# Performance work log

Hardware: AMD Instinct MI355X
Metric: run time of the kernel (lower is better)

## Reference

```python
import jax, jax.numpy as jnp
import numpy as np

T, N, E = 4, 20000, 320000
F_IN, EH, NH, GH, OUT = 12, 32, 64, 64, 1
NUM_LAYERS = 2
EB_IN = (EH + 2 * NH) * 2 + GH  # 384
NB_IN = 2 * NH + 2 * EH + GH    # 256
GB_IN = NH + EH + GH            # 160


def setup_inputs() -> dict:
    key = jax.random.key(0)
    ks = jax.random.split(key, 24)
    f32 = jnp.float32
    def w(k, fan_in, shape):
        return jax.random.normal(k, shape, f32) * (1.0 / np.sqrt(fan_in))
    return {
        "node_attr": jax.random.normal(ks[0], (T, N, F_IN), f32),
        "edge_attr": jax.random.normal(ks[1], (T, E, 1), f32),
        "edge_index": jax.random.randint(ks[2], (2, E), 0, N, jnp.int32),
        "sp_L_vals": jax.random.normal(ks[3], (E,), f32),
        "global_attr": jax.random.normal(ks[4], (1, GH), f32),
        "coeff": jnp.full((1,), 0.1, f32),
        "W_ee": w(ks[5], 1, (1, EH)), "b_ee": jnp.zeros((EH,), f32),
        "W_ne": w(ks[6], F_IN, (F_IN, NH)), "b_ne": jnp.zeros((NH,), f32),
        "W_eb": w(ks[7], EB_IN, (EB_IN, EH)), "b_eb": jnp.zeros((EH,), f32),
        "W_nb": w(ks[8], NB_IN, (NB_IN, NH)), "b_nb": jnp.zeros((NH,), f32),
        "W_gb": w(ks[9], GB_IN, (GB_IN, GH)), "b_gb": jnp.zeros((GH,), f32),
        "W_nd1": w(ks[10], NH, (NH, NH)), "b_nd1": jnp.zeros((NH,), f32),
        "W_nd2": w(ks[11], NH, (NH, OUT)), "b_nd2": jnp.zeros((OUT,), f32),
    }


def _forward(node_attr, edge_attr, edge_index, sp_L_vals, global_attr, coeff,
             W_ee, b_ee, W_ne, b_ne, W_eb, b_eb, W_nb, b_nb, W_gb, b_gb,
             W_nd1, b_nd1, W_nd2, b_nd2):
    relu = jax.nn.relu
    s, r = edge_index[0], edge_index[1]
    seg = lambda v, idx: jax.ops.segment_sum(v, idx, num_segments=N)
    c = coeff[0]

    # encoders
    x_enc = relu(node_attr @ W_ne + b_ne)   # [T,N,NH]
    e_enc = relu(edge_attr @ W_ee + b_ee)   # [T,E,EH]

    def run_gn(xT, eT, g0):
        # recurrent GN core over processing steps; hidden (h_x,h_e,h_g) starts at zeros
        def step(carry, inp):
            h_x, h_e, h_g = carry
            x_in, e_in = inp
            gE = jnp.broadcast_to(h_g, (E, GH))
            # EdgeBlock: [edge_in, edge_h, sender_in, sender_h, recv_in, recv_h, global]
            edge_cat = jnp.concatenate(
                [e_in, h_e, x_in[s], h_x[s], x_in[r], h_x[r], gE], axis=-1)
            e_new = relu(edge_cat @ W_eb + b_eb)              # [E,EH]
            sent = seg(e_new, s)                              # scatter_add by sender
            recv = seg(e_new, r)                              # scatter_add by receiver
            gN = jnp.broadcast_to(h_g, (N, GH))
            node_cat = jnp.concatenate([x_in, h_x, sent, recv, gN], axis=-1)
            x_new = relu(node_cat @ W_nb + b_nb)              # [N,NH]
            # GlobalBlock: scatter_mean == plain mean (single graph)
            g_cat = jnp.concatenate(
                [x_new.mean(0, keepdims=True), e_new.mean(0, keepdims=True), h_g], axis=-1)
            g_new = relu(g_cat @ W_gb + b_gb)                 # [1,GH]
            # physics terms (pde='diff'): time derivative = state update,
            # spatial derivative = coeff * (graph-Laplacian action via sp_L edge weights)
            t_der = x_new - h_x
            s_der = c * seg(sp_L_vals[:, None] * (x_new[s] - x_new[r]), r)
            return (x_new, e_new, g_new), (x_new, e_new, g_new, t_der, s_der)
        carry0 = (jnp.zeros((N, NH), jnp.float32), jnp.zeros((E, EH), jnp.float32), g0)
        _, ys = jax.lax.scan(step, carry0, (xT, eT))
        return ys  # xs[T,N,NH], es[T,E,EH], gs[T,1,GH], td[T,N,NH], sd[T,N,NH]

    xs, es, gs, td, sd = run_gn(x_enc, e_enc, global_attr)
    x_pre = x_enc
    for _ in range(NUM_LAYERS - 1):
        x_res = xs + x_pre          # residual node state feeds next GN layer
        x_pre = x_res
        xs, es, gs, td, sd = run_gn(x_res, es, gs[0])

    x_final = xs + x_pre            # add_residual=True final residual
    h = relu(x_final @ W_nd1 + b_nd1)
    out_nodes = h @ W_nd2 + b_nd2   # [T,N,OUT]
    return out_nodes, td, sd


def reference(node_attr, edge_attr, edge_index, sp_L_vals, global_attr, coeff,
              W_ee, b_ee, W_ne, b_ne, W_eb, b_eb, W_nb, b_nb, W_gb, b_gb,
              W_nd1, b_nd1, W_nd2, b_nd2):
    return _forward(node_attr, edge_attr, edge_index, sp_L_vals, global_attr, coeff,
                    W_ee, b_ee, W_ne, b_ne, W_eb, b_eb, W_nb, b_nb, W_gb, b_gb,
                    W_nd1, b_nd1, W_nd2, b_nd2)
```

## Files before the change

kernel.cpp:

```cpp
#include <hip/hip_runtime.h>


typedef __attribute__((ext_vector_type(8))) short s16x8;
typedef __attribute__((ext_vector_type(4))) float f32x4;

#define T_STEPS 4
#define NN 20000
#define NP 20224
#define NE 320000

__device__ __forceinline__ float bf2f(unsigned short h){
  return __uint_as_float(((unsigned)h)<<16);
}
__device__ __forceinline__ unsigned short f2bf(float f){
  unsigned u = __float_as_uint(f);
  return (unsigned short)((u + 0x7fffu + ((u>>16)&1u)) >> 16);
}
__device__ __forceinline__ float loadIn(const void* p, size_t i, int bf){
  return bf ? bf2f(((const unsigned short*)p)[i]) : ((const float*)p)[i];
}
__device__ __forceinline__ void storeOut(void* o, size_t i, float v, int bf){
  if(bf) ((unsigned short*)o)[i] = f2bf(v);
  else   ((float*)o)[i] = v;
}
__device__ __forceinline__ void load8(const float* __restrict__ p, float* v){
  const float4* q4 = (const float4*)p;
  float4 a = q4[0], b = q4[1];
  v[0]=a.x; v[1]=a.y; v[2]=a.z; v[3]=a.w;
  v[4]=b.x; v[5]=b.y; v[6]=b.z; v[7]=b.w;
}
__device__ __forceinline__ int4 pack8(const float* v){
  unsigned p0 = (unsigned)f2bf(v[0]) | ((unsigned)f2bf(v[1])<<16);
  unsigned p1 = (unsigned)f2bf(v[2]) | ((unsigned)f2bf(v[3])<<16);
  unsigned p2 = (unsigned)f2bf(v[4]) | ((unsigned)f2bf(v[5])<<16);
  unsigned p3 = (unsigned)f2bf(v[6]) | ((unsigned)f2bf(v[7])<<16);
  return make_int4((int)p0,(int)p1,(int)p2,(int)p3);
}
__device__ __forceinline__ void unp8(int4 w, float* a){
  unsigned x;
  x=(unsigned)w.x; a[0]=__uint_as_float(x<<16); a[1]=__uint_as_float(x&0xffff0000u);
  x=(unsigned)w.y; a[2]=__uint_as_float(x<<16); a[3]=__uint_as_float(x&0xffff0000u);
  x=(unsigned)w.z; a[4]=__uint_as_float(x<<16); a[5]=__uint_as_float(x&0xffff0000u);
  x=(unsigned)w.w; a[6]=__uint_as_float(x<<16); a[7]=__uint_as_float(x&0xffff0000u);
}

union I4S8 { int4 i; s16x8 s; };

struct ConvJob { const void* src; float* dst; int n; };
struct ConvJobs { ConvJob j[16]; int cnt; };

__global__ void conv_kernel(ConvJobs jobs, const void* coeff_in, int* flagp,
                            float* coeff_f, float* z, int zn){
  unsigned short u = ((const unsigned short*)coeff_in)[0];
  float as_bf = bf2f(u);
  int bf = (fabsf(as_bf - 0.1f) < 0.02f) ? 1 : 0;
  int tid = blockIdx.x*blockDim.x + threadIdx.x;
  if(tid==0){ *flagp = bf; *coeff_f = bf ? as_bf : ((const float*)coeff_in)[0]; }
  int stride = gridDim.x*blockDim.x;
  for(int q=0;q<jobs.cnt;q++){
    const void* s = jobs.j[q].src; float* d = jobs.j[q].dst; int n = jobs.j[q].n;
    for(int i=tid;i<n;i+=stride) d[i] = loadIn(s, i, bf);
  }
  for(int i=tid;i<zn;i+=stride) z[i]=0.f;
}

__global__ void csr_hist(const int* __restrict__ ei, int* deg_s, int* deg_r,
                         unsigned short* __restrict__ rank_s,
                         unsigned short* __restrict__ rank_r){
  int e = blockIdx.x*256+threadIdx.x;
  rank_s[e] = (unsigned short)atomicAdd(&deg_s[ei[e]],1);
  rank_r[e] = (unsigned short)atomicAdd(&deg_r[ei[NE+e]],1);
}

__global__ void csr_scan(const int* __restrict__ deg_s, int* __restrict__ off_s,
                         const int* __restrict__ deg_r, int* __restrict__ off_r){
  const int CH = NP/256;
  const int* deg = blockIdx.x ? deg_r : deg_s;
  int* off = blockIdx.x ? off_r : off_s;
  int t = threadIdx.x;
  int base = t*CH;
  int s = 0;
  #pragma unroll 8
  for(int i=0;i<CH;i++) s += deg[base+i];
  int lane = t & 63, w = t >> 6;
  int x = s;
  #pragma unroll
  for(int o=1;o<64;o<<=1){
    int y = __shfl_up(x, o, 64);
    if(lane >= o) x += y;
  }
  __shared__ int wtot[4];
  if(lane==63) wtot[w] = x;
  __syncthreads();
  int wbase = 0;
  #pragma unroll
  for(int k=0;k<3;k++) if(k<w) wbase += wtot[k];
  int acc = wbase + x - s;
  #pragma unroll 8
  for(int i=0;i<CH;i++){
    off[base+i]=acc; acc+=deg[base+i];
  }
  if(t==255) off[NN]=acc;
}

__global__ void fill_pack_enc_kernel(
  const int* __restrict__ ei,
  const int* __restrict__ s_off, const int* __restrict__ r_off,
  const unsigned short* __restrict__ rank_s,
  const unsigned short* __restrict__ rank_r,
  int* __restrict__ csr_s, int* __restrict__ csr_r, int2* __restrict__ sr2,
  const void* __restrict__ spL, float* __restrict__ spL_p,
  const void* __restrict__ W_eb_in, const void* __restrict__ W_nb_in,
  const void* __restrict__ W_nd1_in,
  unsigned short* __restrict__ WpE, unsigned short* __restrict__ WpN,
  unsigned short* __restrict__ WpD, unsigned short* __restrict__ WpP,
  const void* __restrict__ na, const float* __restrict__ W_ne,
  const float* __restrict__ b_ne, unsigned short* __restrict__ xA,
  const int* flagp)
{
  __shared__ float arow[4][12];
  const int blk = blockIdx.x;
  const int bf = *flagp;
  if(blk < NE/256){
    int e = blk*256+threadIdx.x;
    int s = ei[e], r = ei[NE+e];
    int p = r_off[r] + rank_r[e];
    sr2[p] = make_int2(s,r);
    csr_r[p] = e;
    csr_s[s_off[s]+rank_s[e]] = p;
    spL_p[p] = loadIn(spL, e, bf);
  } else if(blk < NE/256 + 120){
    int idx = (blk - NE/256)*256 + threadIdx.x;
    if(idx < 22528){
      const void* W; unsigned short* P; int KW, NT;
      if(idx < 2048){ W=W_eb_in; P=WpE; KW=2; NT=2; }
      else if(idx < 18432){ idx -= 2048; W=W_nb_in; P=WpN; KW=8; NT=4; }
      else { idx -= 18432; W=W_nd1_in; P=WpD; KW=2; NT=4; }
      int j = idx & 7;
      int lane = (idx>>3) & 63;
      int rest = idx >> 9;
      int kw = rest % KW;
      int nt = rest / KW;
      int k = kw*32 + (lane>>4)*8 + j;
      int n = nt*16 + (lane&15);
      P[idx] = f2bf(loadIn(W, (size_t)k*(NT*16) + n, bf));
    } else {
      int idx2 = idx - 22528;
      int j = idx2 & 7;
      int lane = (idx2>>3) & 63;
      int rest = idx2 >> 9;
      int kw = rest & 3;
      int nt = rest >> 2;
      int row = (nt<2 ? 64 : 192) + kw*32 + (lane>>4)*8 + j;
      int col = (nt&1)*16 + (lane&15);
      WpP[idx2] = f2bf(loadIn(W_eb_in, (size_t)row*32 + col, bf));
    }
  } else {
    int lane = threadIdx.x & 63, nl = threadIdx.x >> 6;
    int row = (blk - (NE/256 + 120))*4 + nl;
    if(lane<12) arow[nl][lane] = loadIn(na, (size_t)row*12+lane, bf);
    __syncthreads();
    float acc = b_ne[lane];
    #pragma unroll
    for(int k=0;k<12;k++) acc += arow[nl][k]*W_ne[k*64+lane];
    xA[(size_t)row*64+lane] = f2bf(fmaxf(acc,0.f));
  }
}

__global__ __launch_bounds__(256) void node_pre_kernel(
  const unsigned short* __restrict__ x_in,
  const unsigned short* __restrict__ h_x,
  const unsigned short* __restrict__ WpP,
  const float* __restrict__ g,
  const void* __restrict__ W_eb_in, const float* __restrict__ b_eb,
  float* __restrict__ srT, float* __restrict__ gbias,
  const int* flagp)
{
  const int tid = threadIdx.x, lane = tid&63;
  const int q = lane>>4, m16 = lane&15;
  if(blockIdx.x >= 313){
    if(tid < 32){
      int bf = *flagp;
      float gb = b_eb[tid];
      for(int k=0;k<64;k++){
        float gv = bf2f(f2bf(g[k]));
        float wv = bf2f(f2bf(loadIn(W_eb_in, (size_t)(320+k)*32 + tid, bf)));
        gb += gv*wv;
      }
      gbias[tid] = gb;
    }
    return;
  }
  const int tile = blockIdx.x*4 + (tid>>6);
  if(tile >= NN/16) return;
  const int n0 = tile*16, ng = n0+m16;
  const int4 z4 = make_int4(0,0,0,0);
  I4S8 A[4];
  { const int4* xp = (const int4*)(x_in + (size_t)ng*64);
    A[0].i = xp[q]; A[1].i = xp[4+q]; }
  if(h_x){ const int4* hp = (const int4*)(h_x + (size_t)ng*64);
    A[2].i = hp[q]; A[3].i = hp[4+q];
  } else { A[2].i = z4; A[3].i = z4; }
  f32x4 acc[4];
  #pragma unroll
  for(int nt=0;nt<4;nt++) acc[nt] = (f32x4){0.f,0.f,0.f,0.f};
  #pragma unroll
  for(int kw=0;kw<4;kw++){
    #pragma unroll
    for(int nt=0;nt<4;nt++){
      s16x8 b = *(const s16x8*)(WpP + (size_t)((nt*4+kw)*64 + lane)*8);
      acc[nt] = __builtin_amdgcn_mfma_f32_16x16x32_bf16(A[kw].s, b, acc[nt], 0,0,0);
    }
  }
  #pragma unroll
  for(int r=0;r<4;r++){
    int n = n0 + q*4 + r;
    #pragma unroll
    for(int nt=0;nt<4;nt++)
      srT[(size_t)n*64 + nt*16 + m16] = acc[nt][r];
  }
}

__global__ __launch_bounds__(256) void edge_block_mfma(
  const int2* __restrict__ sr2,
  const void* __restrict__ e_attr,
  int e_attr_off,
  const int* __restrict__ inv,
  const unsigned short* __restrict__ e_in,
  const unsigned short* __restrict__ h_e,
  const float* __restrict__ W_ee, const float* __restrict__ b_ee,
  const unsigned short* __restrict__ Wp,
  const float* __restrict__ srT,
  const float* __restrict__ gbias,
  unsigned short* __restrict__ e_out,
  float* __restrict__ partial_e,
  const int* flagp)
{
  const int tid = threadIdx.x;
  const int lane = tid&63;
  const int q = lane>>4, m16 = lane&15;
  const int pair = blockIdx.x*4 + (tid>>6);
  const int e0 = pair*32;
  const int eg0 = e0 + m16, eg1 = e0 + 16 + m16;
  const int o8 = q*8;
  const int4 z4 = make_int4(0,0,0,0);

  I4S8 A0[2], A1[2];
  if(e_attr){
    int bf = *flagp;
    float a0v = loadIn(e_attr, (size_t)e_attr_off + inv[eg0], bf);
    float a1v = loadIn(e_attr, (size_t)e_attr_off + inv[eg1], bf);
    float v[8];
    #pragma unroll
    for(int j=0;j<8;j++) v[j] = fmaxf(a0v*W_ee[o8+j]+b_ee[o8+j], 0.f);
    A0[0].i = pack8(v);
    #pragma unroll
    for(int j=0;j<8;j++) v[j] = fmaxf(a1v*W_ee[o8+j]+b_ee[o8+j], 0.f);
    A1[0].i = pack8(v);
  } else {
    A0[0].i = ((const int4*)(e_in + (size_t)eg0*32))[q];
    A1[0].i = ((const int4*)(e_in + (size_t)eg1*32))[q];
  }
  A0[1].i = h_e ? ((const int4*)(h_e + (size_t)eg0*32))[q] : z4;
  A1[1].i = h_e ? ((const int4*)(h_e + (size_t)eg1*32))[q] : z4;

  f32x4 a00={0.f,0.f,0.f,0.f}, a01={0.f,0.f,0.f,0.f};
  f32x4 a10={0.f,0.f,0.f,0.f}, a11={0.f,0.f,0.f,0.f};
  #pragma unroll
  for(int kw=0;kw<2;kw++){
    s16x8 b0 = *(const s16x8*)(Wp + (size_t)(kw*64 + lane)*8);
    s16x8 b1 = *(const s16x8*)(Wp + (size_t)((2+kw)*64 + lane)*8);
    a00 = __builtin_amdgcn_mfma_f32_16x16x32_bf16(A0[kw].s, b0, a00, 0,0,0);
    a01 = __builtin_amdgcn_mfma_f32_16x16x32_bf16(A0[kw].s, b1, a01, 0,0,0);
    a10 = __builtin_amdgcn_mfma_f32_16x16x32_bf16(A1[kw].s, b0, a10, 0,0,0);
    a11 = __builtin_amdgcn_mfma_f32_16x16x32_bf16(A1[kw].s, b1, a11, 0,0,0);
  }

  const float gb0 = gbias[m16], gb1 = gbias[16+m16];
  int2 rw[8];
  #pragma unroll
  for(int r=0;r<4;r++){
    rw[r]   = sr2[e0 + q*4 + r];
    rw[4+r] = sr2[e0 + 16 + q*4 + r];
  }
  float sv0[8], sv1[8], rv0[8], rv1[8];
  #pragma unroll
  for(int k=0;k<8;k++){
    sv0[k] = srT[(size_t)rw[k].x*64 + m16];
    sv1[k] = srT[(size_t)rw[k].x*64 + 16 + m16];
    rv0[k] = srT[(size_t)rw[k].y*64 + 32 + m16];
    rv1[k] = srT[(size_t)rw[k].y*64 + 48 + m16];
  }

  float pe0=0.f, pe1=0.f;
  #pragma unroll
  for(int r=0;r<4;r++){
    int eg0m = e0 + q*4 + r;
    int eg1m = eg0m + 16;
    float v00 = fmaxf(a00[r] + sv0[r]   + rv0[r]   + gb0, 0.f);
    float v01 = fmaxf(a01[r] + sv1[r]   + rv1[r]   + gb1, 0.f);
    float v10 = fmaxf(a10[r] + sv0[4+r] + rv0[4+r] + gb0, 0.f);
    float v11 = fmaxf(a11[r] + sv1[4+r] + rv1[4+r] + gb1, 0.f);
    e_out[(size_t)eg0m*32+m16]    = f2bf(v00);
    e_out[(size_t)eg0m*32+16+m16] = f2bf(v01);
    e_out[(size_t)eg1m*32+m16]    = f2bf(v10);
    e_out[(size_t)eg1m*32+16+m16] = f2bf(v11);
    pe0 += v00+v10; pe1 += v01+v11;
  }
  pe0 += __shfl_xor(pe0,16,64); pe0 += __shfl_xor(pe0,32,64);
  pe1 += __shfl_xor(pe1,16,64); pe1 += __shfl_xor(pe1,32,64);
  if(q==0){
    int slot = blockIdx.x & 63;
    atomicAdd(&partial_e[slot*32+m16],    pe0);
    atomicAdd(&partial_e[slot*32+16+m16], pe1);
  }
}

__global__ void aggregate_kernel(const unsigned short* __restrict__ e_new,
  const int* __restrict__ s_off, const int* __restrict__ csr_s,
  const int* __restrict__ r_off,
  unsigned short* __restrict__ sentB, unsigned short* __restrict__ recvB)
{
  int node = blockIdx.x*4 + (threadIdx.x>>6);
  int lane = threadIdx.x & 63;
  int c4 = (lane & 7) * 4;
  int jr = lane >> 3;
  float s0=0.f,s1=0.f,s2=0.f,s3=0.f;
  float r0=0.f,r1=0.f,r2=0.f,r3=0.f;
  {
    int beg = s_off[node], end = s_off[node+1];
    for(int i=beg+jr; i<end; i+=8){
      uint2 w = *(const uint2*)(e_new + (size_t)csr_s[i]*32 + c4);
      s0 += __uint_as_float(w.x<<16);
      s1 += __uint_as_float(w.x&0xffff0000u);
      s2 += __uint_as_float(w.y<<16);
      s3 += __uint_as_float(w.y&0xffff0000u);
    }
  }
  {
    int beg = r_off[node], end = r_off[node+1];
    for(int i=beg+jr; i<end; i+=8){
      uint2 w = *(const uint2*)(e_new + (size_t)i*32 + c4);
      r0 += __uint_as_float(w.x<<16);
      r1 += __uint_as_float(w.x&0xffff0000u);
      r2 += __uint_as_float(w.y<<16);
      r3 += __uint_as_float(w.y&0xffff0000u);
    }
  }
  #pragma unroll
  for(int o=8;o<64;o<<=1){
    s0 += __shfl_xor(s0,o,64); s1 += __shfl_xor(s1,o,64);
    s2 += __shfl_xor(s2,o,64); s3 += __shfl_xor(s3,o,64);
    r0 += __shfl_xor(r0,o,64); r1 += __shfl_xor(r1,o,64);
    r2 += __shfl_xor(r2,o,64); r3 += __shfl_xor(r3,o,64);
  }
  if(jr==0){
    unsigned slo = (unsigned)f2bf(s0) | ((unsigned)f2bf(s1)<<16);
    unsigned shi = (unsigned)f2bf(s2) | ((unsigned)f2bf(s3)<<16);
    unsigned rlo = (unsigned)f2bf(r0) | ((unsigned)f2bf(r1)<<16);
    unsigned rhi = (unsigned)f2bf(r2) | ((unsigned)f2bf(r3)<<16);
    *(uint2*)(sentB + (size_t)node*32 + c4) = make_uint2(slo,shi);
    *(uint2*)(recvB + (size_t)node*32 + c4) = make_uint2(rlo,rhi);
  }
}

__global__ __launch_bounds__(256) void node_block_mfma(
  const unsigned short* __restrict__ x_in, const unsigned short* __restrict__ h_x,
  const unsigned short* __restrict__ sentB, const unsigned short* __restrict__ recvB,
  const float* __restrict__ g,
  const unsigned short* __restrict__ Wp,
  const float* __restrict__ b_nb,
  unsigned short* __restrict__ x_out,
  unsigned short* __restrict__ xres_out,
  float* __restrict__ partial_x,
  void* __restrict__ out_base, size_t td_off, int has_td,
  float* __restrict__ partial_e,
  const float* __restrict__ W_gb, const float* __restrict__ b_gb,
  float* __restrict__ g_out, int* __restrict__ cnt,
  const int* flagp)
{
  __shared__ int lastFlag;
  __shared__ float gcat[160];
  __shared__ float red[4][64];
  const int tid = threadIdx.x, lane = tid&63;
  const int q = lane>>4, m16 = lane&15;
  const int tile = blockIdx.x*4 + (tid>>6);
  if(tile < NN/16){
    const int n0 = tile*16;
    const int ng = n0+m16;
    const int o8 = q*8;
    const int4 z4 = make_int4(0,0,0,0);

    I4S8 A[8];
    { const int4* xp = (const int4*)(x_in + (size_t)ng*64);
      A[0].i = xp[q]; A[1].i = xp[4+q]; }
    if(h_x){ const int4* hp = (const int4*)(h_x + (size_t)ng*64);
      A[2].i = hp[q]; A[3].i = hp[4+q];
    } else { A[2].i = z4; A[3].i = z4; }
    A[4].i = ((const int4*)(sentB + (size_t)ng*32))[q];
    A[5].i = ((const int4*)(recvB + (size_t)ng*32))[q];
    { float v[8];
      load8(g + o8, v);      A[6].i = pack8(v);
      load8(g + 32 + o8, v); A[7].i = pack8(v); }

    f32x4 acc[4];
    #pragma unroll
    for(int nt=0;nt<4;nt++) acc[nt] = (f32x4){0.f,0.f,0.f,0.f};
    #pragma unroll
    for(int kw=0;kw<8;kw++){
      #pragma unroll
      for(int nt=0;nt<4;nt++){
        s16x8 b = *(const s16x8*)(Wp + (size_t)((nt*8+kw)*64 + lane)*8);
        acc[nt] = __builtin_amdgcn_mfma_f32_16x16x32_bf16(A[kw].s, b, acc[nt], 0,0,0);
      }
    }

    int bf = has_td ? *flagp : 0;
    float ps[4] = {0.f,0.f,0.f,0.f};
    #pragma unroll
    for(int r=0;r<4;r++){
      int nodeg = n0 + q*4 + r;
      #pragma unroll
      for(int nt=0;nt<4;nt++){
        int col = nt*16 + m16;
        float vv = fmaxf(acc[nt][r] + b_nb[col], 0.f);
        unsigned short hb = f2bf(vv);
        x_out[(size_t)nodeg*64+col] = hb;
        if(xres_out){
          float xv = bf2f(x_in[(size_t)nodeg*64+col]);
          xres_out[(size_t)nodeg*64+col] = f2bf(xv + bf2f(hb));
        }
        if(has_td){
          float hxv = h_x ? bf2f(h_x[(size_t)nodeg*64+col]) : 0.f;
          storeOut(out_base, td_off + (size_t)nodeg*64+col, vv - hxv, bf);
        }
        ps[nt] += vv;
      }
    }
    #pragma unroll
    for(int nt=0;nt<4;nt++){
      ps[nt] += __shfl_xor(ps[nt],16,64);
      ps[nt] += __shfl_xor(ps[nt],32,64);
    }
    if(q==0){
      int slot = blockIdx.x & 63;
      #pragma unroll
      for(int nt=0;nt<4;nt++)
        atomicAdd(&partial_x[slot*64 + nt*16 + m16], ps[nt]);
    }
  }

  asm volatile("s_waitcnt vmcnt(0)" ::: "memory");
  __syncthreads();
  if(tid==0) lastFlag = (atomicAdd(cnt,1) == (int)gridDim.x - 1) ? 1 : 0;
  __syncthreads();
  if(!lastFlag) return;

  if(tid<64){
    float sx = 0.f;
    #pragma unroll 8
    for(int i=0;i<64;i++)
      sx += __hip_atomic_load(&partial_x[i*64+tid], __ATOMIC_RELAXED, __HIP_MEMORY_SCOPE_AGENT);
    gcat[tid] = sx * (1.0f/(float)NN);
  } else if(tid<96){
    int j = tid-64;
    float se = 0.f;
    #pragma unroll 8
    for(int i=0;i<64;i++)
      se += __hip_atomic_load(&partial_e[i*32+j], __ATOMIC_RELAXED, __HIP_MEMORY_SCOPE_AGENT);
    gcat[64+j] = se * (1.0f/(float)NE);
  } else if(tid<160){
    gcat[tid] = g[tid-96];
  }
  __syncthreads();
  int j = tid&63, cc = tid>>6;
  float acc2 = 0.f;
  #pragma unroll 8
  for(int k=cc*40;k<cc*40+40;k++) acc2 += gcat[k]*W_gb[k*64+j];
  red[cc][j] = acc2;
  __syncthreads();
  for(int i=tid;i<2048;i+=256) partial_e[i]=0.f;
  for(int i=tid;i<4096;i+=256) partial_x[i]=0.f;
  if(tid<64){
    float a = red[0][tid]+red[1][tid]+red[2][tid]+red[3][tid] + b_gb[tid];
    g_out[tid] = fmaxf(a, 0.f);
  }
  if(tid==0) *cnt = 0;
}

__global__ void sder_csr_kernel(const int2* __restrict__ sr2,
  const float* __restrict__ spL_p, const unsigned short* __restrict__ x_new,
  const int* __restrict__ r_off,
  const float* __restrict__ coeff, void* __restrict__ out_base, size_t off,
  const int* flagp)
{
  int bf = *flagp;
  int lane = threadIdx.x&63, nl = threadIdx.x>>6;
  int node = blockIdx.x*4+nl;
  float xn = bf2f(x_new[(size_t)node*64+lane]);
  float a0=0.f, a1=0.f, a2=0.f, a3=0.f;
  int beg = r_off[node], end = r_off[node+1];
  int i = beg;
  for(; i+4<=end; i+=4){
    float w1 = spL_p[i],   w2 = spL_p[i+1];
    float w3 = spL_p[i+2], w4 = spL_p[i+3];
    int s1 = sr2[i].x, s2 = sr2[i+1].x, s3 = sr2[i+2].x, s4 = sr2[i+3].x;
    a0 += w1*(bf2f(x_new[(size_t)s1*64+lane])-xn);
    a1 += w2*(bf2f(x_new[(size_t)s2*64+lane])-xn);
    a2 += w3*(bf2f(x_new[(size_t)s3*64+lane])-xn);
    a3 += w4*(bf2f(x_new[(size_t)s4*64+lane])-xn);
  }
  for(; i<end; i++){
    float w1 = spL_p[i];
    a0 += w1*(bf2f(x_new[(size_t)sr2[i].x*64+lane])-xn);
  }
  storeOut(out_base, off + (size_t)node*64+lane, coeff[0]*((a0+a1)+(a2+a3)), bf);
}

__global__ __launch_bounds__(256) void decoder_kernel(
  const unsigned short* __restrict__ xs, const unsigned short* __restrict__ xr,
  const unsigned short* __restrict__ WpD,
  const float* __restrict__ b1, const float* __restrict__ W2,
  const float* __restrict__ b2,
  void* __restrict__ out_base, const int* flagp)
{
  const int tid=threadIdx.x, lane=tid&63;
  const int q=lane>>4, m16=lane&15;
  const int tile = blockIdx.x*4 + (tid>>6);
  const int row0 = tile*16;
  const int rg = row0 + m16;

  I4S8 A[2];
  #pragma unroll
  for(int kw=0;kw<2;kw++){
    int4 xa = ((const int4*)(xs + (size_t)rg*64 + kw*32))[q];
    int4 xb = ((const int4*)(xr + (size_t)rg*64 + kw*32))[q];
    float va[8], vb[8], v[8];
    unp8(xa, va); unp8(xb, vb);
    #pragma unroll
    for(int j=0;j<8;j++) v[j] = va[j]+vb[j];
    A[kw].i = pack8(v);
  }

  f32x4 acc[4];
  #pragma unroll
  for(int nt=0;nt<4;nt++) acc[nt] = (f32x4){0.f,0.f,0.f,0.f};
  #pragma unroll
  for(int kw=0;kw<2;kw++){
    #pragma unroll
    for(int nt=0;nt<4;nt++){
      s16x8 b = *(const s16x8*)(WpD + (size_t)((nt*2+kw)*64 + lane)*8);
      acc[nt] = __builtin_amdgcn_mfma_f32_16x16x32_bf16(A[kw].s, b, acc[nt], 0,0,0);
    }
  }

  float val[4];
  #pragma unroll
  for(int r=0;r<4;r++){
    float s = 0.f;
    #pragma unroll
    for(int nt=0;nt<4;nt++){
      int col = nt*16 + m16;
      s += fmaxf(acc[nt][r] + b1[col], 0.f) * W2[col];
    }
    val[r] = s;
  }
  #pragma unroll
  for(int o=1;o<16;o<<=1){
    #pragma unroll
    for(int r=0;r<4;r++) val[r] += __shfl_xor(val[r], o, 64);
  }
  if(m16==0){
    int bf = *flagp;
    float bb = b2[0];
    #pragma unroll
    for(int r=0;r<4;r++)
      storeOut(out_base, (size_t)(row0 + q*4 + r), val[r] + bb, bf);
  }
}

extern "C" void kernel_launch(void* const* d_in, const int* in_sizes, int n_in,
                              void* d_out, int out_size, void* d_ws, size_t ws_size,
                              hipStream_t stream){
  const void* node_attr = d_in[0];
  const void* edge_attr = d_in[1];
  const int*  ei        = (const int*)d_in[2];
  const void* spL       = d_in[3];
  const void* gattr     = d_in[4];
  const void* coeff_in  = d_in[5];
  const void* W_ee_in = d_in[6];  const void* b_ee_in = d_in[7];
  const void* W_ne_in = d_in[8];  const void* b_ne_in = d_in[9];
  const void* W_eb_in = d_in[10]; const void* b_eb_in = d_in[11];
  const void* W_nb_in = d_in[12]; const void* b_nb_in = d_in[13];
  const void* W_gb_in = d_in[14]; const void* b_gb_in = d_in[15];
  const void* W_nd1_in= d_in[16]; const void* b_nd1_in= d_in[17];
  const void* W_nd2_in= d_in[18]; const void* b_nd2_in= d_in[19];

  float* ws = (float*)d_ws;
  float* W_ee_f = ws;             float* b_ee_f = W_ee_f+32;
  float* W_ne_f = b_ee_f+32;      float* b_ne_f = W_ne_f+768;
  float* W_gb_f = b_ne_f+64;      float* b_gb_f = W_gb_f+10240;
  float* W_nd1_f= b_gb_f+64;      float* b_nd1_f= W_nd1_f+4096;
  float* W_nd2_f= b_nd1_f+64;     float* b_nd2_f= W_nd2_f+64;
  float* b_eb_f = b_nd2_f+1;      float* b_nb_f = b_eb_f+32;
  float* coeff_f= b_nb_f+64;
  int*   flagp  = (int*)(ws + 15523);
  float* gbuf   = ws + 15524;
  float* zbase  = ws + 16100;
  int*   cnt    = (int*)zbase;
  float* part_e = zbase + 4;
  float* part_x = part_e + 2048;
  int*   deg_s  = (int*)(part_x + 4096);
  int*   deg_r  = deg_s + NP;
  int*   s_off  = deg_r + NP;
  int*   r_off  = s_off + NP+1;
  unsigned short* rank_s = (unsigned short*)(r_off + NP+1);
  unsigned short* rank_r = rank_s + NE;
  int*   csr_s  = (int*)(rank_r + NE);
  int*   csr_r  = csr_s + NE;
  float* spL_p  = (float*)(csr_r + NE);
  size_t iend   = (size_t)((int*)(spL_p + NE) - (int*)ws);
  iend = (iend + 3) & ~(size_t)3;
  int2*  sr2    = (int2*)(ws + iend);
  unsigned short* sentB = (unsigned short*)(sr2 + NE);
  unsigned short* recvB = sentB + (size_t)NN*32;
  unsigned short* eBuf  = recvB + (size_t)NN*32;
  unsigned short* xA    = eBuf + (size_t)T_STEPS*NE*32;
  unsigned short* xB    = xA + (size_t)T_STEPS*NN*64;
  unsigned short* xC    = xB + (size_t)T_STEPS*NN*64;
  unsigned short* WpE   = xC + (size_t)T_STEPS*NN*64;
  unsigned short* WpN   = WpE + 2048;
  unsigned short* WpD   = WpN + 16384;
  unsigned short* WpP   = WpD + 4096;
  float* srT   = (float*)(WpP + 8192);
  float* gbias = srT + (size_t)NN*64;

  ConvJobs jobs; int c=0;
  auto add=[&](const void* s, float* d, int n){ jobs.j[c].src=s; jobs.j[c].dst=d; jobs.j[c].n=n; c++; };
  add(W_ee_in,W_ee_f,32);   add(b_ee_in,b_ee_f,32);
  add(W_ne_in,W_ne_f,768);  add(b_ne_in,b_ne_f,64);
  add(W_gb_in,W_gb_f,10240);add(b_gb_in,b_gb_f,64);
  add(W_nd1_in,W_nd1_f,4096);add(b_nd1_in,b_nd1_f,64);
  add(W_nd2_in,W_nd2_f,64); add(b_nd2_in,b_nd2_f,1);
  add(b_eb_in,b_eb_f,32);   add(b_nb_in,b_nb_f,64);
  add(gattr,gbuf,64);
  jobs.cnt=c;
  conv_kernel<<<64,256,0,stream>>>(jobs, coeff_in, flagp, coeff_f,
      zbase, 4+2048+4096+2*NP);

  csr_hist<<<NE/256,256,0,stream>>>(ei, deg_s, deg_r, rank_s, rank_r);
  csr_scan<<<2,256,0,stream>>>(deg_s, s_off, deg_r, r_off);

  fill_pack_enc_kernel<<<NE/256 + 120 + T_STEPS*NN/4,256,0,stream>>>(
      ei, s_off, r_off, rank_s, rank_r, csr_s, csr_r, sr2, spL, spL_p,
      W_eb_in, W_nb_in, W_nd1_in, WpE, WpN, WpD, WpP,
      node_attr, W_ne_f, b_ne_f, xA, flagp);

  const size_t td_base = (size_t)T_STEPS*NN;
  const size_t sd_base = td_base + (size_t)T_STEPS*NN*64;

  for(int layer=0; layer<2; layer++){
    for(int t=0;t<T_STEPS;t++){
      const unsigned short* x_in = (layer==0? xA : xC) + (size_t)t*NN*64;
      const unsigned short* h_x  = (t>0)? xB + (size_t)(t-1)*NN*64 : nullptr;
      const unsigned short* h_e  = (t>0)? eBuf + (size_t)(t-1)*NE*32 : nullptr;
      const float* gptr = (layer==0)? gbuf + t*64
                                    : (t==0? gbuf+1*64 : gbuf+(4+t)*64);
      float*       gout = (layer==0)? gbuf+(1+t)*64 : gbuf+(5+t)*64;
      const void*  eat  = (layer==0)? edge_attr : nullptr;
      const unsigned short* e_in = (layer==0)? nullptr : eBuf + (size_t)t*NE*32;
      unsigned short*       e_out= eBuf + (size_t)t*NE*32;

      node_pre_kernel<<<314,256,0,stream>>>(x_in, h_x, WpP, gptr,
          W_eb_in, b_eb_f, srT, gbias, flagp);

      edge_block_mfma<<<NE/128,256,0,stream>>>(sr2, eat, t*NE, csr_r,
          e_in, h_e, W_ee_f, b_ee_f, WpE, srT, gbias, e_out, part_e, flagp);

      aggregate_kernel<<<NN/4,256,0,stream>>>(e_out, s_off, csr_s, r_off,
          sentB, recvB);

      unsigned short* x_out = xB + (size_t)t*NN*64;
      unsigned short* xres  = (layer==0)? xC + (size_t)t*NN*64 : nullptr;
      size_t td_off = td_base + (size_t)t*NN*64;
      node_block_mfma<<<(NN/16+3)/4,256,0,stream>>>(x_in, h_x, sentB, recvB, gptr,
          WpN, b_nb_f, x_out, xres, part_x, d_out, td_off, (layer==1)?1:0,
          part_e, W_gb_f, b_gb_f, gout, cnt, flagp);

      if(layer==1){
        sder_csr_kernel<<<NN/4,256,0,stream>>>(sr2, spL_p, x_out, r_off,
            coeff_f, d_out, sd_base + (size_t)t*NN*64, flagp);
      }
    }
  }

  decoder_kernel<<<(T_STEPS*NN/16+3)/4,256,0,stream>>>(xB, xC, WpD,
      b_nd1_f, W_nd2_f, b_nd2_f, d_out, flagp);
}
```

Measured before the change: 764.7 us.

## Fuse next-step node precompute into node block and widen aggregate loads

Folds the per-step node_pre work (the projection of next-step x_in and the new h_x through WpP, plus the global-bias term) into the tail of node_block_mfma, so node_pre_kernel now launches only at t==0. The new h_x tile is staged through LDS and reused as MFMA input without a round trip to global memory. The aggregate kernel now loads 16-byte vectors with 16 edges in flight per node instead of 8-byte loads over 8 edges. Node_block also gets a launch_bounds occupancy hint. Together this cuts kernel launches and re-reads of node data, but node_block carries more LDS and registers and gains an extra block-wide barrier.

```diff
diff --git a/kernel.cpp b/kernel.cpp
--- a/kernel.cpp
+++ b/kernel.cpp
@@ -323,48 +323,54 @@
 {
   int node = blockIdx.x*4 + (threadIdx.x>>6);
   int lane = threadIdx.x & 63;
-  int c4 = (lane & 7) * 4;
-  int jr = lane >> 3;
-  float s0=0.f,s1=0.f,s2=0.f,s3=0.f;
-  float r0=0.f,r1=0.f,r2=0.f,r3=0.f;
+  int c8 = (lane & 3) * 8;
+  int jr = lane >> 2;
+  float s[8] = {0.f,0.f,0.f,0.f,0.f,0.f,0.f,0.f};
+  float r[8] = {0.f,0.f,0.f,0.f,0.f,0.f,0.f,0.f};
   {
     int beg = s_off[node], end = s_off[node+1];
-    for(int i=beg+jr; i<end; i+=8){
-      uint2 w = *(const uint2*)(e_new + (size_t)csr_s[i]*32 + c4);
-      s0 += __uint_as_float(w.x<<16);
-      s1 += __uint_as_float(w.x&0xffff0000u);
-      s2 += __uint_as_float(w.y<<16);
-      s3 += __uint_as_float(w.y&0xffff0000u);
+    for(int i=beg+jr; i<end; i+=16){
+      uint4 w = *(const uint4*)(e_new + (size_t)csr_s[i]*32 + c8);
+      s[0] += __uint_as_float(w.x<<16); s[1] += __uint_as_float(w.x&0xffff0000u);
+      s[2] += __uint_as_float(w.y<<16); s[3] += __uint_as_float(w.y&0xffff0000u);
+      s[4] += __uint_as_float(w.z<<16); s[5] += __uint_as_float(w.z&0xffff0000u);
+      s[6] += __uint_as_float(w.w<<16); s[7] += __uint_as_float(w.w&0xffff0000u);
     }
   }
   {
     int beg = r_off[node], end = r_off[node+1];
-    for(int i=beg+jr; i<end; i+=8){
-      uint2 w = *(const uint2*)(e_new + (size_t)i*32 + c4);
-      r0 += __uint_as_float(w.x<<16);
-      r1 += __uint_as_float(w.x&0xffff0000u);
-      r2 += __uint_as_float(w.y<<16);
-      r3 += __uint_as_float(w.y&0xffff0000u);
-    }
-  }
-  #pragma unroll
-  for(int o=8;o<64;o<<=1){
-    s0 += __shfl_xor(s0,o,64); s1 += __shfl_xor(s1,o,64);
-    s2 += __shfl_xor(s2,o,64); s3 += __shfl_xor(s3,o,64);
-    r0 += __shfl_xor(r0,o,64); r1 += __shfl_xor(r1,o,64);
-    r2 += __shfl_xor(r2,o,64); r3 += __shfl_xor(r3,o,64);
+    for(int i=beg+jr; i<end; i+=16){
+      uint4 w = *(const uint4*)(e_new + (size_t)i*32 + c8);
+      r[0] += __uint_as_float(w.x<<16); r[1] += __uint_as_float(w.x&0xffff0000u);
+      r[2] += __uint_as_float(w.y<<16); r[3] += __uint_as_float(w.y&0xffff0000u);
+      r[4] += __uint_as_float(w.z<<16); r[5] += __uint_as_float(w.z&0xffff0000u);
+      r[6] += __uint_as_float(w.w<<16); r[7] += __uint_as_float(w.w&0xffff0000u);
+    }
+  }
+  #pragma unroll
+  for(int o=4;o<64;o<<=1){
+    #pragma unroll
+    for(int k=0;k<8;k++){
+      s[k] += __shfl_xor(s[k],o,64);
+      r[k] += __shfl_xor(r[k],o,64);
+    }
   }
   if(jr==0){
-    unsigned slo = (unsigned)f2bf(s0) | ((unsigned)f2bf(s1)<<16);
-    unsigned shi = (unsigned)f2bf(s2) | ((unsigned)f2bf(s3)<<16);
-    unsigned rlo = (unsigned)f2bf(r0) | ((unsigned)f2bf(r1)<<16);
-    unsigned rhi = (unsigned)f2bf(r2) | ((unsigned)f2bf(r3)<<16);
-    *(uint2*)(sentB + (size_t)node*32 + c4) = make_uint2(slo,shi);
-    *(uint2*)(recvB + (size_t)node*32 + c4) = make_uint2(rlo,rhi);
-  }
-}
-
-__global__ __launch_bounds__(256) void node_block_mfma(
+    uint4 ws, wr;
+    ws.x = (unsigned)f2bf(s[0]) | ((unsigned)f2bf(s[1])<<16);
+    ws.y = (unsigned)f2bf(s[2]) | ((unsigned)f2bf(s[3])<<16);
+    ws.z = (unsigned)f2bf(s[4]) | ((unsigned)f2bf(s[5])<<16);
+    ws.w = (unsigned)f2bf(s[6]) | ((unsigned)f2bf(s[7])<<16);
+    wr.x = (unsigned)f2bf(r[0]) | ((unsigned)f2bf(r[1])<<16);
+    wr.y = (unsigned)f2bf(r[2]) | ((unsigned)f2bf(r[3])<<16);
+    wr.z = (unsigned)f2bf(r[4]) | ((unsigned)f2bf(r[5])<<16);
+    wr.w = (unsigned)f2bf(r[6]) | ((unsigned)f2bf(r[7])<<16);
+    *(uint4*)(sentB + (size_t)node*32 + c8) = ws;
+    *(uint4*)(recvB + (size_t)node*32 + c8) = wr;
+  }
+}
+
+__global__ __launch_bounds__(256,4) void node_block_mfma(
   const unsigned short* __restrict__ x_in, const unsigned short* __restrict__ h_x,
   const unsigned short* __restrict__ sentB, const unsigned short* __restrict__ recvB,
   const float* __restrict__ g,
@@ -377,17 +383,25 @@
   float* __restrict__ partial_e,
   const float* __restrict__ W_gb, const float* __restrict__ b_gb,
   float* __restrict__ g_out, int* __restrict__ cnt,
+  const unsigned short* __restrict__ x_next,
+  const unsigned short* __restrict__ WpP,
+  float* __restrict__ srT,
+  const void* __restrict__ W_eb_in, const float* __restrict__ b_eb,
+  float* __restrict__ gbias_out,
   const int* flagp)
 {
   __shared__ int lastFlag;
   __shared__ float gcat[160];
   __shared__ float red[4][64];
+  __shared__ __align__(16) unsigned short hlds[4][16][80];
   const int tid = threadIdx.x, lane = tid&63;
   const int q = lane>>4, m16 = lane&15;
-  const int tile = blockIdx.x*4 + (tid>>6);
-  if(tile < NN/16){
-    const int n0 = tile*16;
-    const int ng = n0+m16;
+  const int w = tid>>6;
+  const int tile = blockIdx.x*4 + w;
+  const int n0 = tile*16;
+  const int ng = n0+m16;
+  const bool active = (tile < NN/16);
+  if(active){
     const int o8 = q*8;
     const int4 z4 = make_int4(0,0,0,0);
 
@@ -426,6 +440,7 @@
         float vv = fmaxf(acc[nt][r] + b_nb[col], 0.f);
         unsigned short hb = f2bf(vv);
         x_out[(size_t)nodeg*64+col] = hb;
+        hlds[w][q*4+r][col] = hb;
         if(xres_out){
           float xv = bf2f(x_in[(size_t)nodeg*64+col]);
           xres_out[(size_t)nodeg*64+col] = f2bf(xv + bf2f(hb));
@@ -447,6 +462,33 @@
       #pragma unroll
       for(int nt=0;nt<4;nt++)
         atomicAdd(&partial_x[slot*64 + nt*16 + m16], ps[nt]);
+    }
+  }
+
+  __syncthreads();
+  if(x_next && active){
+    I4S8 P[4];
+    { const int4* xp = (const int4*)(x_next + (size_t)ng*64);
+      P[0].i = xp[q]; P[1].i = xp[4+q]; }
+    P[2].i = *(const int4*)&hlds[w][m16][8*q];
+    P[3].i = *(const int4*)&hlds[w][m16][32+8*q];
+    f32x4 accp[4];
+    #pragma unroll
+    for(int nt=0;nt<4;nt++) accp[nt] = (f32x4){0.f,0.f,0.f,0.f};
+    #pragma unroll
+    for(int kw=0;kw<4;kw++){
+      #pragma unroll
+      for(int nt=0;nt<4;nt++){
+        s16x8 b = *(const s16x8*)(WpP + (size_t)((nt*4+kw)*64 + lane)*8);
+        accp[nt] = __builtin_amdgcn_mfma_f32_16x16x32_bf16(P[kw].s, b, accp[nt], 0,0,0);
+      }
+    }
+    #pragma unroll
+    for(int r=0;r<4;r++){
+      int n = n0 + q*4 + r;
+      #pragma unroll
+      for(int nt=0;nt<4;nt++)
+        srT[(size_t)n*64 + nt*16 + m16] = accp[nt][r];
     }
   }
 
@@ -481,11 +523,25 @@
   __syncthreads();
   for(int i=tid;i<2048;i+=256) partial_e[i]=0.f;
   for(int i=tid;i<4096;i+=256) partial_x[i]=0.f;
+  float gv_out = 0.f;
   if(tid<64){
     float a = red[0][tid]+red[1][tid]+red[2][tid]+red[3][tid] + b_gb[tid];
-    g_out[tid] = fmaxf(a, 0.f);
+    gv_out = fmaxf(a, 0.f);
+    g_out[tid] = gv_out;
+    gcat[tid] = gv_out;
   }
   if(tid==0) *cnt = 0;
+  __syncthreads();
+  if(gbias_out && tid<32){
+    int bf = *flagp;
+    float gb = b_eb[tid];
+    for(int k=0;k<64;k++){
+      float gv = bf2f(f2bf(gcat[k]));
+      float wv = bf2f(f2bf(loadIn(W_eb_in, (size_t)(320+k)*32 + tid, bf)));
+      gb += gv*wv;
+    }
+    gbias_out[tid] = gb;
+  }
 }
 
 __global__ void sder_csr_kernel(const int2* __restrict__ sr2,
@@ -671,8 +727,10 @@
       const unsigned short* e_in = (layer==0)? nullptr : eBuf + (size_t)t*NE*32;
       unsigned short*       e_out= eBuf + (size_t)t*NE*32;
 
-      node_pre_kernel<<<314,256,0,stream>>>(x_in, h_x, WpP, gptr,
-          W_eb_in, b_eb_f, srT, gbias, flagp);
+      if(t==0){
+        node_pre_kernel<<<314,256,0,stream>>>(x_in, h_x, WpP, gptr,
+            W_eb_in, b_eb_f, srT, gbias, flagp);
+      }
 
       edge_block_mfma<<<NE/128,256,0,stream>>>(sr2, eat, t*NE, csr_r,
           e_in, h_e, W_ee_f, b_ee_f, WpE, srT, gbias, e_out, part_e, flagp);
@@ -683,9 +741,12 @@
       unsigned short* x_out = xB + (size_t)t*NN*64;
       unsigned short* xres  = (layer==0)? xC + (size_t)t*NN*64 : nullptr;
       size_t td_off = td_base + (size_t)t*NN*64;
+      const unsigned short* x_next = (t<T_STEPS-1)
+          ? ((layer==0? xA : xC) + (size_t)(t+1)*NN*64) : nullptr;
       node_block_mfma<<<(NN/16+3)/4,256,0,stream>>>(x_in, h_x, sentB, recvB, gptr,
           WpN, b_nb_f, x_out, xres, part_x, d_out, td_off, (layer==1)?1:0,
-          part_e, W_gb_f, b_gb_f, gout, cnt, flagp);
+          part_e, W_gb_f, b_gb_f, gout, cnt,
+          x_next, WpP, srT, W_eb_in, b_eb_f, gbias, flagp);
 
       if(layer==1){
         sder_csr_kernel<<<NN/4,256,0,stream>>>(sr2, spL_p, x_out, r_off,
```

Result: slower. 817.0 us (+6.8%).
